# Kernel tuning notes

Hardware: AMD Instinct MI355X
Metric: run time of the kernel (lower is better)

The kernel has to match this reference:

```python
import jax, jax.numpy as jnp
import numpy as np

TAO = 1.0
EPS = 1e-8


def setup_inputs() -> dict:
    key = jax.random.key(0)
    k1, k2, k3 = jax.random.split(key, 3)
    B, S, H = 32, 64, 256
    tmap = jax.random.normal(k1, (B, S, S, H), dtype=jnp.float32)
    pos_query = jax.random.normal(k2, (B, H), dtype=jnp.float32)
    r = jax.random.uniform(k3, (B, S, S))
    mask2d_pos = r < 0.05
    mask2d_neg = (r >= 0.05) & (r < 0.35)
    return {"pos_query": pos_query, "tmap": tmap,
            "mask2d_pos": mask2d_pos, "mask2d_neg": mask2d_neg}


def reference(pos_query, tmap, mask2d_pos, mask2d_neg):
    # Original loops over batch, gathers variable-length pos/neg sets, normalizes
    # twice (once without eps, once with eps inside sim()), then InfoNCE-style loss.
    # Vectorized: compute similarities for ALL (i,j) cells once, reduce with masks.
    u = tmap / jnp.linalg.norm(tmap, axis=-1, keepdims=True)          # pos/neg normalize (no eps)
    u = u / (jnp.linalg.norm(u, axis=-1, keepdims=True) + EPS)        # renormalize inside sim() (with eps)
    q = pos_query / (jnp.linalg.norm(pos_query, axis=-1, keepdims=True) + EPS)
    s = jnp.einsum('bijh,bh->bij', u, q)                              # cosine sims (B,S,S)
    e = jnp.exp(s / TAO)
    num = jnp.sum(e * mask2d_pos, axis=(1, 2))                        # sum exp(pos_sim/tao)
    den = num + jnp.sum(e * mask2d_neg, axis=(1, 2))                  # + sum exp(neg_sim/tao)
    li = -jnp.log(num / (den + EPS))                                  # per-sample loss (B,)
    # original skips samples with empty pos or neg set, averages over the rest
    valid = jnp.any(mask2d_pos, axis=(1, 2)) & jnp.any(mask2d_neg, axis=(1, 2))
    n_valid = jnp.maximum(jnp.sum(valid), 1)
    return jnp.sum(jnp.where(valid, li, 0.0)) / n_valid
```

## Files before the change

### kernel.cpp

```cpp
#include <hip/hip_runtime.h>
#include <math.h>

#define EPSF 1e-8f
constexpr int B = 32;
constexpr int S = 64;
constexpr int H = 256;
constexpr int H4 = H / 4;
constexpr int CELLS_PER_BATCH = S * S;
constexpr int CELLS = B * CELLS_PER_BATCH;
constexpr int CELLS_PER_WAVE = 8;
constexpr int WAVES_PER_BLOCK = 4;
constexpr int CELLS_PER_BLOCK = CELLS_PER_WAVE * WAVES_PER_BLOCK;

#define WS_ACC_BASE 64
#define WS_ACC_STRIDE 32
#define WS_NEG_OFF 16

__global__ __launch_bounds__(64) void prep_kernel(const float* __restrict__ pq,
                                                  float* __restrict__ ws) {
    int b = blockIdx.x;
    int lane = threadIdx.x;
    float4 v = ((const float4*)pq)[b * H4 + lane];
    float ss = v.x * v.x + v.y * v.y + v.z * v.z + v.w * v.w;
    #pragma unroll
    for (int off = 32; off > 0; off >>= 1) ss += __shfl_xor(ss, off);
    if (lane == 0) {
        ws[b] = 1.0f / (sqrtf(ss) + EPSF);
        ws[WS_ACC_BASE + b * WS_ACC_STRIDE] = 0.0f;
        ws[WS_ACC_BASE + b * WS_ACC_STRIDE + WS_NEG_OFF] = 0.0f;
    }
}

__global__ __launch_bounds__(256) void main_kernel(const float* __restrict__ tmap,
                                                   const float* __restrict__ pq,
                                                   const int* __restrict__ mask_pos,
                                                   const int* __restrict__ mask_neg,
                                                   float* __restrict__ ws) {
    int tid = threadIdx.x;
    int lane = tid & 63;
    int wid = tid >> 6;
    int cellBase = blockIdx.x * CELLS_PER_BLOCK + wid * CELLS_PER_WAVE;
    int b = cellBase >> 12;

    float4 q4 = ((const float4*)pq)[b * H4 + lane];
    float scale = ws[b] * (1.0f / (1.0f + EPSF));

    float wp = 0.0f, wn = 0.0f;
    #pragma unroll
    for (int k = 0; k < CELLS_PER_WAVE; ++k) {
        int cell = cellBase + k;
        float4 t = ((const float4*)tmap)[cell * H4 + lane];
        float d  = t.x * q4.x + t.y * q4.y + t.z * q4.z + t.w * q4.w;
        float ss = t.x * t.x + t.y * t.y + t.z * t.z + t.w * t.w;
        #pragma unroll
        for (int off = 32; off > 0; off >>= 1) {
            d  += __shfl_xor(d, off);
            ss += __shfl_xor(ss, off);
        }
        float s = d * scale * rsqrtf(ss);
        float e = __expf(s);
        if (mask_pos[cell] != 0) wp += e;
        if (mask_neg[cell] != 0) wn += e;
    }

    __shared__ float sp[WAVES_PER_BLOCK], sn[WAVES_PER_BLOCK];
    if (lane == 0) { sp[wid] = wp; sn[wid] = wn; }
    __syncthreads();
    if (tid == 0) {
        float tp = 0.0f, tn = 0.0f;
        #pragma unroll
        for (int w = 0; w < WAVES_PER_BLOCK; ++w) { tp += sp[w]; tn += sn[w]; }
        atomicAdd(&ws[WS_ACC_BASE + b * WS_ACC_STRIDE], tp);
        atomicAdd(&ws[WS_ACC_BASE + b * WS_ACC_STRIDE + WS_NEG_OFF], tn);
    }
}

__global__ __launch_bounds__(64) void final_kernel(const float* __restrict__ ws,
                                                   float* __restrict__ out) {
    int lane = threadIdx.x;
    float li = 0.0f;
    int v = 0;
    if (lane < B) {
        float ep = ws[WS_ACC_BASE + lane * WS_ACC_STRIDE];
        float en = ws[WS_ACC_BASE + lane * WS_ACC_STRIDE + WS_NEG_OFF];
        if (ep > 0.0f && en > 0.0f) {
            v = 1;
            li = -logf(ep / (ep + en + EPSF));
        }
    }
    #pragma unroll
    for (int off = 32; off > 0; off >>= 1) {
        li += __shfl_xor(li, off);
        v  += __shfl_xor(v, off);
    }
    if (lane == 0) out[0] = li / (float)(v > 0 ? v : 1);
}

extern "C" void kernel_launch(void* const* d_in, const int* in_sizes, int n_in,
                              void* d_out, int out_size, void* d_ws, size_t ws_size,
                              hipStream_t stream) {
    const float* pos_query = (const float*)d_in[0];
    const float* tmap      = (const float*)d_in[1];
    const int*   mask_pos  = (const int*)d_in[2];
    const int*   mask_neg  = (const int*)d_in[3];
    float* out = (float*)d_out;
    float* ws  = (float*)d_ws;

    prep_kernel<<<B, 64, 0, stream>>>(pos_query, ws);
    main_kernel<<<CELLS / CELLS_PER_BLOCK, 256, 0, stream>>>(tmap, pos_query,
                                                             mask_pos, mask_neg, ws);
    final_kernel<<<1, 64, 0, stream>>>(ws, out);
}
```

Baseline: 199.9 us.

## Drop prep kernel, replace atomics with per-block partials, vectorize mask loads

Removes the prep kernel by having each wave compute the query norm inline. The per-batch atomic accumulation is replaced with per-block partial sums, which a wider final kernel reduces hierarchically. Mask values are loaded as int4 vectors up front, and each wave now handles twice as many cells, halving the block count. This saves one launch and avoids atomic contention, at the cost of some redundant query-norm work in every wave.

```diff
diff --git a/kernel.cpp b/kernel.cpp
--- a/kernel.cpp
+++ b/kernel.cpp
@@ -8,28 +8,12 @@
 constexpr int H4 = H / 4;
 constexpr int CELLS_PER_BATCH = S * S;
 constexpr int CELLS = B * CELLS_PER_BATCH;
-constexpr int CELLS_PER_WAVE = 8;
+constexpr int CELLS_PER_WAVE = 16;
 constexpr int WAVES_PER_BLOCK = 4;
 constexpr int CELLS_PER_BLOCK = CELLS_PER_WAVE * WAVES_PER_BLOCK;
+constexpr int NBLK = CELLS / CELLS_PER_BLOCK;
+constexpr int BLOCKS_PER_BATCH = NBLK / B;
 
-#define WS_ACC_BASE 64
-#define WS_ACC_STRIDE 32
-#define WS_NEG_OFF 16
-
-__global__ __launch_bounds__(64) void prep_kernel(const float* __restrict__ pq,
-                                                  float* __restrict__ ws) {
-    int b = blockIdx.x;
-    int lane = threadIdx.x;
-    float4 v = ((const float4*)pq)[b * H4 + lane];
-    float ss = v.x * v.x + v.y * v.y + v.z * v.z + v.w * v.w;
-    #pragma unroll
-    for (int off = 32; off > 0; off >>= 1) ss += __shfl_xor(ss, off);
-    if (lane == 0) {
-        ws[b] = 1.0f / (sqrtf(ss) + EPSF);
-        ws[WS_ACC_BASE + b * WS_ACC_STRIDE] = 0.0f;
-        ws[WS_ACC_BASE + b * WS_ACC_STRIDE + WS_NEG_OFF] = 0.0f;
-    }
-}
 
 __global__ __launch_bounds__(256) void main_kernel(const float* __restrict__ tmap,
                                                    const float* __restrict__ pq,
@@ -43,7 +27,19 @@
     int b = cellBase >> 12;
 
     float4 q4 = ((const float4*)pq)[b * H4 + lane];
-    float scale = ws[b] * (1.0f / (1.0f + EPSF));
+    float qss = q4.x * q4.x + q4.y * q4.y + q4.z * q4.z + q4.w * q4.w;
+    #pragma unroll
+    for (int off = 32; off > 0; off >>= 1) qss += __shfl_xor(qss, off);
+    float scale = (1.0f / (sqrtf(qss) + EPSF)) * (1.0f / (1.0f + EPSF));
+
+    int mp[CELLS_PER_WAVE], mn[CELLS_PER_WAVE];
+    #pragma unroll
+    for (int v = 0; v < CELLS_PER_WAVE / 4; ++v) {
+        int4 a = ((const int4*)(mask_pos + cellBase))[v];
+        int4 c = ((const int4*)(mask_neg + cellBase))[v];
+        mp[v*4+0] = a.x; mp[v*4+1] = a.y; mp[v*4+2] = a.z; mp[v*4+3] = a.w;
+        mn[v*4+0] = c.x; mn[v*4+1] = c.y; mn[v*4+2] = c.z; mn[v*4+3] = c.w;
+    }
 
     float wp = 0.0f, wn = 0.0f;
     #pragma unroll
@@ -59,8 +55,8 @@
         }
         float s = d * scale * rsqrtf(ss);
         float e = __expf(s);
-        if (mask_pos[cell] != 0) wp += e;
-        if (mask_neg[cell] != 0) wn += e;
+        if (mp[k] != 0) wp += e;
+        if (mn[k] != 0) wn += e;
     }
 
     __shared__ float sp[WAVES_PER_BLOCK], sn[WAVES_PER_BLOCK];
@@ -70,30 +66,51 @@
         float tp = 0.0f, tn = 0.0f;
         #pragma unroll
         for (int w = 0; w < WAVES_PER_BLOCK; ++w) { tp += sp[w]; tn += sn[w]; }
-        atomicAdd(&ws[WS_ACC_BASE + b * WS_ACC_STRIDE], tp);
-        atomicAdd(&ws[WS_ACC_BASE + b * WS_ACC_STRIDE + WS_NEG_OFF], tn);
+        ws[blockIdx.x * 2]     = tp;
+        ws[blockIdx.x * 2 + 1] = tn;
     }
 }
 
-__global__ __launch_bounds__(64) void final_kernel(const float* __restrict__ ws,
-                                                   float* __restrict__ out) {
-    int lane = threadIdx.x;
-    float li = 0.0f;
-    int v = 0;
-    if (lane < B) {
-        float ep = ws[WS_ACC_BASE + lane * WS_ACC_STRIDE];
-        float en = ws[WS_ACC_BASE + lane * WS_ACC_STRIDE + WS_NEG_OFF];
+__global__ __launch_bounds__(256) void final_kernel(const float* __restrict__ ws,
+                                                    float* __restrict__ out) {
+    int tid = threadIdx.x;
+    int batch = tid >> 3;
+    int sub = tid & 7;
+
+    float ep = 0.0f, en = 0.0f;
+    #pragma unroll
+    for (int j = 0; j < BLOCKS_PER_BATCH / 8; ++j) {
+        int blk = batch * BLOCKS_PER_BATCH + sub * (BLOCKS_PER_BATCH / 8) + j;
+        ep += ws[blk * 2];
+        en += ws[blk * 2 + 1];
+    }
+    #pragma unroll
+    for (int off = 1; off < 8; off <<= 1) {
+        ep += __shfl_xor(ep, off);
+        en += __shfl_xor(en, off);
+    }
+
+    __shared__ float lli[B];
+    __shared__ int   lv[B];
+    if (sub == 0) {
+        int v = 0; float li = 0.0f;
         if (ep > 0.0f && en > 0.0f) {
             v = 1;
             li = -logf(ep / (ep + en + EPSF));
         }
+        lli[batch] = li; lv[batch] = v;
     }
-    #pragma unroll
-    for (int off = 32; off > 0; off >>= 1) {
-        li += __shfl_xor(li, off);
-        v  += __shfl_xor(v, off);
+    __syncthreads();
+    if (tid < 64) {
+        float li = (tid < B) ? lli[tid] : 0.0f;
+        int   v  = (tid < B) ? lv[tid]  : 0;
+        #pragma unroll
+        for (int off = 32; off > 0; off >>= 1) {
+            li += __shfl_xor(li, off);
+            v  += __shfl_xor(v, off);
+        }
+        if (tid == 0) out[0] = li / (float)(v > 0 ? v : 1);
     }
-    if (lane == 0) out[0] = li / (float)(v > 0 ? v : 1);
 }
 
 extern "C" void kernel_launch(void* const* d_in, const int* in_sizes, int n_in,
@@ -106,8 +123,6 @@
     float* out = (float*)d_out;
     float* ws  = (float*)d_ws;
 
-    prep_kernel<<<B, 64, 0, stream>>>(pos_query, ws);
-    main_kernel<<<CELLS / CELLS_PER_BLOCK, 256, 0, stream>>>(tmap, pos_query,
-                                                             mask_pos, mask_neg, ws);
-    final_kernel<<<1, 64, 0, stream>>>(ws, out);
+    main_kernel<<<NBLK, 256, 0, stream>>>(tmap, pos_query, mask_pos, mask_neg, ws);
+    final_kernel<<<1, 256, 0, stream>>>(ws, out);
 }
```

After: 202.3 us. No clear change (+1.2%).
